# Kernel tuning notes

Measured on AMD Instinct MI355X. Metric: run time of the kernel, lower is better.

The kernel has to match this reference:

```python
import jax, jax.numpy as jnp
import numpy as np

WS = 4      # window_size
H = 128     # hidden_size
IN = 3      # input_size (1 control + 2 state channels)
OUT = 2     # out_size = input_size - 1


def _lstm_layer(x, Wih, Whh, b):
    # x: [B, S, Din] -> ys: [B, S, H], h/c: [B, H]. PyTorch gate order i,f,g,o.
    B = x.shape[0]
    xg = jnp.einsum('bsd,gd->bsg', x, Wih) + b  # precompute input projections

    def step(carry, xt):
        h, c = carry
        g = xt + h @ Whh.T
        i, f, gg, o = jnp.split(g, 4, axis=-1)
        c = jax.nn.sigmoid(f) * c + jax.nn.sigmoid(i) * jnp.tanh(gg)
        h = jax.nn.sigmoid(o) * jnp.tanh(c)
        return (h, c), h

    z = jnp.zeros((B, Whh.shape[1]), x.dtype)
    (h, c), ys = jax.lax.scan(step, (z, z), xg.transpose(1, 0, 2))
    return ys.transpose(1, 0, 2), h, c


def _lstm2(x, p):
    (Wih0, Whh0, b0), (Wih1, Whh1, b1) = p
    y0, h0, c0 = _lstm_layer(x, Wih0, Whh0, b0)
    y1, h1, c1 = _lstm_layer(y0, Wih1, Whh1, b1)
    return y1, jnp.stack([h0, h1]), jnp.stack([c0, c1])


def _forward(traj, Wih0, Whh0, bih0, bhh0, Wih1, Whh1, bih1, bhh1, Wl, bl):
    p = ((Wih0, Whh0, bih0 + bhh0), (Wih1, Whh1, bih1 + bhh1))
    head = lambda ys: ys[:, -1] @ Wl.T + bl  # linear applied to last LSTM step (== pred[:, -1])
    T = traj.shape[1]

    # initial window on raw trajectory
    ys, h, c = _lstm2(traj[:, :WS], p)
    out = traj[:, WS - 1:WS, 1:] + head(ys)[:, None, :]  # [B, 1, OUT]

    # warm-up phase: windows mix raw traj rows with predicted rows (features ordered [ctrl, out])
    for t in range(1, WS):
        tmp = jnp.concatenate([traj[:, WS + t:WS + t + 1, 0:1], out[:, t - 1:t, :]], axis=2)
        seq = jnp.concatenate([traj[:, t:WS + t - 1, :], tmp], axis=1)  # [B, WS, IN]
        ys, h, c = _lstm2(seq, p)
        out = jnp.concatenate([out, traj[:, WS + t - 1:WS + t, 1:] + head(ys)[:, None, :]], axis=1)

    nsteps = T - 2 * WS
    idx = WS + np.arange(nsteps)[:, None] + np.arange(WS)[None, :]  # [nsteps, WS]
    ctrl = traj[:, :, 0][:, idx].transpose(1, 0, 2)[..., None]      # [nsteps, B, WS, 1]

    def step(carry, ctrl_t):
        win, _, _ = carry
        seq = jnp.concatenate([win, ctrl_t], axis=2)  # [B, WS, OUT+1]
        ys, h, c = _lstm2(seq, p)
        new = win[:, -1, :] + head(ys)                # [B, OUT]
        win = jnp.concatenate([win[:, 1:], new[:, None, :]], axis=1)
        return (win, h, c), new

    (win, h, c), news = jax.lax.scan(step, (out, h, c), ctrl)
    out = jnp.concatenate([out, news.transpose(1, 0, 2)], axis=1)  # [B, T-WS, OUT]
    return out, h, c


def setup_inputs():
    key = jax.random.key(0)
    ks = jax.random.split(key, 11)
    B, T = 128, 256
    s = 1.0 / np.sqrt(H)
    u = lambda k, shp: jax.random.uniform(k, shp, jnp.float32, -s, s)
    return dict(
        one_full_traj=jax.random.normal(ks[0], (B, T, IN), jnp.float32),
        Wih0=u(ks[1], (4 * H, IN)), Whh0=u(ks[2], (4 * H, H)),
        bih0=u(ks[3], (4 * H,)), bhh0=u(ks[4], (4 * H,)),
        Wih1=u(ks[5], (4 * H, H)), Whh1=u(ks[6], (4 * H, H)),
        bih1=u(ks[7], (4 * H,)), bhh1=u(ks[8], (4 * H,)),
        Wl=u(ks[9], (OUT, H)), bl=u(ks[10], (OUT,)),
    )


def reference(one_full_traj, Wih0, Whh0, bih0, bhh0, Wih1, Whh1, bih1, bhh1, Wl, bl):
    # returns (out, h_n, c_n) matching torch's (out, hidden)
    return _forward(one_full_traj, Wih0, Whh0, bih0, bhh0, Wih1, Whh1, bih1, bhh1, Wl, bl)
```

## Files before the change

### kernel.cpp

```cpp
#include <hip/hip_runtime.h>

typedef _Float16 half2_t __attribute__((ext_vector_type(2)));
typedef unsigned int u32;

#define NW 252

__device__ inline u32 pk(float x, float y) {
  half2_t h; h.x = (_Float16)x; h.y = (_Float16)y;
  return __builtin_bit_cast(u32, h);
}

__device__ inline float fdot2(u32 a, u32 b, float c) {
#if __has_builtin(__builtin_amdgcn_fdot2)
  return __builtin_amdgcn_fdot2(__builtin_bit_cast(half2_t, a),
                                __builtin_bit_cast(half2_t, b), c, false);
#else
  half2_t ah = __builtin_bit_cast(half2_t, a);
  half2_t bh = __builtin_bit_cast(half2_t, b);
  return c + (float)ah.x * (float)bh.x + (float)ah.y * (float)bh.y;
#endif
}

__device__ inline float fast_rcp(float x) {
#if __has_builtin(__builtin_amdgcn_rcpf)
  return __builtin_amdgcn_rcpf(x);
#else
  return 1.0f / x;
#endif
}

__device__ inline float sigf(float x)  { return fast_rcp(1.0f + __expf(-x)); }
__device__ inline float tanh_(float x) { return 1.0f - 2.0f * fast_rcp(__expf(2.0f * x) + 1.0f); }

__device__ inline float quad_reduce(float v) {
  int x = __builtin_bit_cast(int, v);
  int y = __builtin_amdgcn_update_dpp(0, x, 0xB1, 0xF, 0xF, true);
  v += __builtin_bit_cast(float, y);
  x = __builtin_bit_cast(int, v);
  y = __builtin_amdgcn_update_dpp(0, x, 0x4E, 0xF, 0xF, true);
  v += __builtin_bit_cast(float, y);
  return v;
}

#define LOAD_SLICE(dst, basehalf)                                          \
  { const uint4* _p = (const uint4*)(basehalf) + ks * 4;                   \
    uint4 _q0 = _p[0], _q1 = _p[1], _q2 = _p[2], _q3 = _p[3];              \
    dst[0]=_q0.x;  dst[1]=_q0.y;  dst[2]=_q0.z;  dst[3]=_q0.w;             \
    dst[4]=_q1.x;  dst[5]=_q1.y;  dst[6]=_q1.z;  dst[7]=_q1.w;             \
    dst[8]=_q2.x;  dst[9]=_q2.y;  dst[10]=_q2.z; dst[11]=_q2.w;            \
    dst[12]=_q3.x; dst[13]=_q3.y; dst[14]=_q3.z; dst[15]=_q3.w; }

__global__ __launch_bounds__(512) void lstm_roll(
    const float* __restrict__ traj,
    const float* __restrict__ Wih0, const float* __restrict__ Whh0,
    const float* __restrict__ bih0, const float* __restrict__ bhh0,
    const float* __restrict__ Wih1, const float* __restrict__ Whh1,
    const float* __restrict__ bih1, const float* __restrict__ bhh1,
    const float* __restrict__ Wl,   const float* __restrict__ bl,
    float* __restrict__ out)
{
  const int b   = blockIdx.x;
  const int B   = gridDim.x;
  const int tid = threadIdx.x;
  const int j   = tid >> 2;
  const int ks  = tid & 3;

  __shared__ __align__(16) _Float16 h0buf[2][128];
  __shared__ __align__(16) _Float16 h1buf[2][128];
  __shared__ float sh_h1f[128];
  __shared__ float sh_Wl[256];
  __shared__ float trajS[256 * 3];
  __shared__ float preds[NW * 2];

  for (int i = tid; i < 768; i += 512) trajS[i] = traj[b * 768 + i];
  if (tid < 256) sh_Wl[tid] = Wl[tid];
  float blv = 0.0f;
  if (tid < 128) blv = bl[tid >> 6];

  u32 wA[64], wB[64], wC[64];
  float b0r[4], b1r[4], w0r[12];
#pragma unroll
  for (int g = 0; g < 4; ++g) {
    const int row = g * 128 + j;
    b0r[g] = bih0[row] + bhh0[row];
    b1r[g] = bih1[row] + bhh1[row];
    w0r[g*3+0] = Wih0[row*3+0];
    w0r[g*3+1] = Wih0[row*3+1];
    w0r[g*3+2] = Wih0[row*3+2];
    const float4* pA = (const float4*)(Whh0 + row * 128 + ks * 32);
    const float4* pB = (const float4*)(Wih1 + row * 128 + ks * 32);
    const float4* pC = (const float4*)(Whh1 + row * 128 + ks * 32);
#pragma unroll
    for (int q = 0; q < 8; ++q) {
      float4 fa = pA[q], fb = pB[q], fc = pC[q];
      wA[g*16 + q*2    ] = pk(fa.x, fa.y);
      wA[g*16 + q*2 + 1] = pk(fa.z, fa.w);
      wB[g*16 + q*2    ] = pk(fb.x, fb.y);
      wB[g*16 + q*2 + 1] = pk(fb.z, fb.w);
      wC[g*16 + q*2    ] = pk(fc.x, fc.y);
      wC[g*16 + q*2 + 1] = pk(fc.z, fc.w);
    }
  }

  float c0 = 0.f, c1 = 0.f, h0f = 0.f, h1f = 0.f;
  __syncthreads();

#pragma unroll 1
  for (int w = 0; w < NW; ++w) {
    c0 = 0.f; c1 = 0.f;
    for (int t = 0; t < 4; ++t) {
      float x0, x1, x2;
      if (w < 4) {
        if (w == 0 || t < 3) {
          const float* r = &trajS[(w + t) * 3];
          x0 = r[0]; x1 = r[1]; x2 = r[2];
        } else {
          x0 = trajS[(4 + w) * 3];
          x1 = preds[(w - 1) * 2];
          x2 = preds[(w - 1) * 2 + 1];
        }
      } else {
        const int s = w - 4;
        x0 = preds[(s + t) * 2];
        x1 = preds[(s + t) * 2 + 1];
        x2 = trajS[(4 + s + t) * 3];
      }
      const int rp = t & 1, wp = rp ^ 1;
      const bool lead = (ks == 0);

      float acc0, acc1, acc2, acc3;
      {
        float a0 = b0r[0] + w0r[0]*x0 + w0r[1] *x1 + w0r[2] *x2;
        float a1 = b0r[1] + w0r[3]*x0 + w0r[4] *x1 + w0r[5] *x2;
        float a2 = b0r[2] + w0r[6]*x0 + w0r[7] *x1 + w0r[8] *x2;
        float a3 = b0r[3] + w0r[9]*x0 + w0r[10]*x1 + w0r[11]*x2;
        acc0 = lead ? a0 : 0.f;  acc1 = lead ? a1 : 0.f;
        acc2 = lead ? a2 : 0.f;  acc3 = lead ? a3 : 0.f;
      }
      if (t > 0) {
        u32 su[16];
        LOAD_SLICE(su, h0buf[rp]);
#pragma unroll
        for (int kk = 0; kk < 16; ++kk) {
          acc0 = fdot2(wA[     kk], su[kk], acc0);
          acc1 = fdot2(wA[16 + kk], su[kk], acc1);
          acc2 = fdot2(wA[32 + kk], su[kk], acc2);
          acc3 = fdot2(wA[48 + kk], su[kk], acc3);
        }
      }
      acc0 = quad_reduce(acc0); acc1 = quad_reduce(acc1);
      acc2 = quad_reduce(acc2); acc3 = quad_reduce(acc3);
      {
        float ig = sigf(acc0), fg = sigf(acc1), gg = tanh_(acc2), og = sigf(acc3);
        c0  = fg * c0 + ig * gg;
        h0f = og * tanh_(c0);
      }
      if (lead) h0buf[wp][j] = (_Float16)h0f;
      __syncthreads();

      acc0 = lead ? b1r[0] : 0.f;  acc1 = lead ? b1r[1] : 0.f;
      acc2 = lead ? b1r[2] : 0.f;  acc3 = lead ? b1r[3] : 0.f;
      {
        u32 sy[16];
        LOAD_SLICE(sy, h0buf[wp]);
#pragma unroll
        for (int kk = 0; kk < 16; ++kk) {
          acc0 = fdot2(wB[     kk], sy[kk], acc0);
          acc1 = fdot2(wB[16 + kk], sy[kk], acc1);
          acc2 = fdot2(wB[32 + kk], sy[kk], acc2);
          acc3 = fdot2(wB[48 + kk], sy[kk], acc3);
        }
      }
      if (t > 0) {
        u32 sh[16];
        LOAD_SLICE(sh, h1buf[rp]);
#pragma unroll
        for (int kk = 0; kk < 16; ++kk) {
          acc0 = fdot2(wC[     kk], sh[kk], acc0);
          acc1 = fdot2(wC[16 + kk], sh[kk], acc1);
          acc2 = fdot2(wC[32 + kk], sh[kk], acc2);
          acc3 = fdot2(wC[48 + kk], sh[kk], acc3);
        }
      }
      acc0 = quad_reduce(acc0); acc1 = quad_reduce(acc1);
      acc2 = quad_reduce(acc2); acc3 = quad_reduce(acc3);
      {
        float ig = sigf(acc0), fg = sigf(acc1), gg = tanh_(acc2), og = sigf(acc3);
        c1  = fg * c1 + ig * gg;
        h1f = og * tanh_(c1);
      }
      if (lead) {
        h1buf[wp][j] = (_Float16)h1f;
        if (t == 3) sh_h1f[j] = h1f;
      }
      if (t == 3) __syncthreads();
    }

    if (tid < 128) {
      const int d = tid >> 6, l = tid & 63;
      float p = sh_Wl[d*128 + 2*l] * sh_h1f[2*l] + sh_Wl[d*128 + 2*l + 1] * sh_h1f[2*l + 1];
      p += __shfl_xor(p, 1);  p += __shfl_xor(p, 2);  p += __shfl_xor(p, 4);
      p += __shfl_xor(p, 8);  p += __shfl_xor(p, 16); p += __shfl_xor(p, 32);
      if (l == 0) {
        float base = (w < 4) ? trajS[(3 + w) * 3 + 1 + d] : preds[(w - 1) * 2 + d];
        preds[w * 2 + d] = base + p + blv;
      }
    }
    __syncthreads();
  }

  for (int i = tid; i < NW * 2; i += 512) out[b * (NW * 2) + i] = preds[i];
  if (ks == 0) {
    const int oh = B * NW * 2;
    const int oc = oh + 2 * B * 128;
    out[oh +            b * 128 + j] = h0f;
    out[oh + B * 128 +  b * 128 + j] = h1f;
    out[oc +            b * 128 + j] = c0;
    out[oc + B * 128 +  b * 128 + j] = c1;
  }
}

extern "C" void kernel_launch(void* const* d_in, const int* in_sizes, int n_in,
                              void* d_out, int out_size, void* d_ws, size_t ws_size,
                              hipStream_t stream) {
  const float* traj = (const float*)d_in[0];
  const float* Wih0 = (const float*)d_in[1];
  const float* Whh0 = (const float*)d_in[2];
  const float* bih0 = (const float*)d_in[3];
  const float* bhh0 = (const float*)d_in[4];
  const float* Wih1 = (const float*)d_in[5];
  const float* Whh1 = (const float*)d_in[6];
  const float* bih1 = (const float*)d_in[7];
  const float* bhh1 = (const float*)d_in[8];
  const float* Wl   = (const float*)d_in[9];
  const float* bl   = (const float*)d_in[10];

  const int B = in_sizes[0] / (256 * 3);
  hipLaunchKernelGGL(lstm_roll, dim3(B), dim3(512), 0, stream,
                     traj, Wih0, Whh0, bih0, bhh0, Wih1, Whh1, bih1, bhh1,
                     Wl, bl, (float*)d_out);
}
```

Measured before the change: 1.560 ms.

## Skew LSTM layers across time steps and defer head to cut barriers

Restructures the per-window loop as a wavefront. Layer-0 step t+1 now runs in the same barrier phase as layer-1 step t, and layer-0 step 0 of the next window is folded into the last phase of the current one. This cuts block-wide barriers per window from six to four. The linear head is moved to 8 threads using a quad reduce and deferred to the start of the next window, taking its separate barrier off the critical path. It also adds launch_bounds(512,2), which caps registers per thread while each thread keeps 192 packed weight registers, so spilling is a risk.

Result: faster. 1.328 ms (-14.9%).

```diff
diff --git a/kernel.cpp b/kernel.cpp
--- a/kernel.cpp
+++ b/kernel.cpp
@@ -50,7 +50,7 @@
     dst[8]=_q2.x;  dst[9]=_q2.y;  dst[10]=_q2.z; dst[11]=_q2.w;            \
     dst[12]=_q3.x; dst[13]=_q3.y; dst[14]=_q3.z; dst[15]=_q3.w; }
 
-__global__ __launch_bounds__(512) void lstm_roll(
+__global__ __launch_bounds__(512, 2) void lstm_roll(
     const float* __restrict__ traj,
     const float* __restrict__ Wih0, const float* __restrict__ Whh0,
     const float* __restrict__ bih0, const float* __restrict__ bhh0,
@@ -75,7 +75,7 @@
   for (int i = tid; i < 768; i += 512) trajS[i] = traj[b * 768 + i];
   if (tid < 256) sh_Wl[tid] = Wl[tid];
   float blv = 0.0f;
-  if (tid < 128) blv = bl[tid >> 6];
+  if (tid < 8) blv = bl[tid >> 2];
 
   u32 wA[64], wB[64], wC[64];
   float b0r[4], b1r[4], w0r[12];
@@ -103,111 +103,130 @@
   }
 
   float c0 = 0.f, c1 = 0.f, h0f = 0.f, h1f = 0.f;
+
+  auto L0STEP = [&](int w_, int t_, int p_) {
+    float x0, x1, x2;
+    if (w_ < 4) {
+      if (w_ == 0 || t_ < 3) {
+        const float* r = &trajS[(w_ + t_) * 3];
+        x0 = r[0]; x1 = r[1]; x2 = r[2];
+      } else {
+        x0 = trajS[(4 + w_) * 3];
+        x1 = preds[(w_ - 1) * 2];
+        x2 = preds[(w_ - 1) * 2 + 1];
+      }
+    } else {
+      const int s_ = w_ - 4;
+      x0 = preds[(s_ + t_) * 2];
+      x1 = preds[(s_ + t_) * 2 + 1];
+      x2 = trajS[(w_ + t_) * 3];
+    }
+    const bool lead = (ks == 0);
+    float a0 = b0r[0] + w0r[0]*x0 + w0r[1] *x1 + w0r[2] *x2;
+    float a1 = b0r[1] + w0r[3]*x0 + w0r[4] *x1 + w0r[5] *x2;
+    float a2 = b0r[2] + w0r[6]*x0 + w0r[7] *x1 + w0r[8] *x2;
+    float a3 = b0r[3] + w0r[9]*x0 + w0r[10]*x1 + w0r[11]*x2;
+    float acc0 = lead ? a0 : 0.f, acc1 = lead ? a1 : 0.f;
+    float acc2 = lead ? a2 : 0.f, acc3 = lead ? a3 : 0.f;
+    if (t_ > 0) {
+      u32 su[16];
+      LOAD_SLICE(su, h0buf[p_]);
+#pragma unroll
+      for (int kk = 0; kk < 16; ++kk) {
+        acc0 = fdot2(wA[     kk], su[kk], acc0);
+        acc1 = fdot2(wA[16 + kk], su[kk], acc1);
+        acc2 = fdot2(wA[32 + kk], su[kk], acc2);
+        acc3 = fdot2(wA[48 + kk], su[kk], acc3);
+      }
+    }
+    acc0 = quad_reduce(acc0); acc1 = quad_reduce(acc1);
+    acc2 = quad_reduce(acc2); acc3 = quad_reduce(acc3);
+    float ig = sigf(acc0), fg = sigf(acc1), gg = tanh_(acc2), og = sigf(acc3);
+    float cp = t_ ? c0 : 0.f;
+    c0  = fg * cp + ig * gg;
+    h0f = og * tanh_(c0);
+    if (lead) h0buf[p_ ^ 1][j] = (_Float16)h0f;
+  };
+
+  auto L1STEP = [&](int t_, int p_) {
+    const bool lead = (ks == 0);
+    float acc0 = lead ? b1r[0] : 0.f, acc1 = lead ? b1r[1] : 0.f;
+    float acc2 = lead ? b1r[2] : 0.f, acc3 = lead ? b1r[3] : 0.f;
+    {
+      u32 sy[16];
+      LOAD_SLICE(sy, h0buf[p_]);
+#pragma unroll
+      for (int kk = 0; kk < 16; ++kk) {
+        acc0 = fdot2(wB[     kk], sy[kk], acc0);
+        acc1 = fdot2(wB[16 + kk], sy[kk], acc1);
+        acc2 = fdot2(wB[32 + kk], sy[kk], acc2);
+        acc3 = fdot2(wB[48 + kk], sy[kk], acc3);
+      }
+    }
+    if (t_ > 0) {
+      u32 sh[16];
+      LOAD_SLICE(sh, h1buf[p_]);
+#pragma unroll
+      for (int kk = 0; kk < 16; ++kk) {
+        acc0 = fdot2(wC[     kk], sh[kk], acc0);
+        acc1 = fdot2(wC[16 + kk], sh[kk], acc1);
+        acc2 = fdot2(wC[32 + kk], sh[kk], acc2);
+        acc3 = fdot2(wC[48 + kk], sh[kk], acc3);
+      }
+    }
+    acc0 = quad_reduce(acc0); acc1 = quad_reduce(acc1);
+    acc2 = quad_reduce(acc2); acc3 = quad_reduce(acc3);
+    float ig = sigf(acc0), fg = sigf(acc1), gg = tanh_(acc2), og = sigf(acc3);
+    float cp = t_ ? c1 : 0.f;
+    c1  = fg * cp + ig * gg;
+    h1f = og * tanh_(c1);
+    if (lead) {
+      h1buf[p_ ^ 1][j] = (_Float16)h1f;
+      if (t_ == 3) sh_h1f[j] = h1f;
+    }
+  };
+
+  auto HD = [&](int w_) {
+    if (tid < 8) {
+      const int d = tid >> 2;
+      const float* wrow = &sh_Wl[d * 128 + ks * 32];
+      const float* hrow = &sh_h1f[ks * 32];
+      float s = 0.f;
+#pragma unroll
+      for (int m = 0; m < 32; ++m) s = fmaf(wrow[m], hrow[m], s);
+      s = quad_reduce(s);
+      if (ks == 0) {
+        float base = (w_ < 4) ? trajS[(3 + w_) * 3 + 1 + d] : preds[(w_ - 1) * 2 + d];
+        preds[w_ * 2 + d] = base + s + blv;
+      }
+    }
+  };
+
   __syncthreads();
+
+  int p = 0;
+  L0STEP(0, 0, p);
+  __syncthreads(); p ^= 1;
 
 #pragma unroll 1
   for (int w = 0; w < NW; ++w) {
-    c0 = 0.f; c1 = 0.f;
-    for (int t = 0; t < 4; ++t) {
-      float x0, x1, x2;
-      if (w < 4) {
-        if (w == 0 || t < 3) {
-          const float* r = &trajS[(w + t) * 3];
-          x0 = r[0]; x1 = r[1]; x2 = r[2];
-        } else {
-          x0 = trajS[(4 + w) * 3];
-          x1 = preds[(w - 1) * 2];
-          x2 = preds[(w - 1) * 2 + 1];
-        }
-      } else {
-        const int s = w - 4;
-        x0 = preds[(s + t) * 2];
-        x1 = preds[(s + t) * 2 + 1];
-        x2 = trajS[(4 + s + t) * 3];
-      }
-      const int rp = t & 1, wp = rp ^ 1;
-      const bool lead = (ks == 0);
-
-      float acc0, acc1, acc2, acc3;
-      {
-        float a0 = b0r[0] + w0r[0]*x0 + w0r[1] *x1 + w0r[2] *x2;
-        float a1 = b0r[1] + w0r[3]*x0 + w0r[4] *x1 + w0r[5] *x2;
-        float a2 = b0r[2] + w0r[6]*x0 + w0r[7] *x1 + w0r[8] *x2;
-        float a3 = b0r[3] + w0r[9]*x0 + w0r[10]*x1 + w0r[11]*x2;
-        acc0 = lead ? a0 : 0.f;  acc1 = lead ? a1 : 0.f;
-        acc2 = lead ? a2 : 0.f;  acc3 = lead ? a3 : 0.f;
-      }
-      if (t > 0) {
-        u32 su[16];
-        LOAD_SLICE(su, h0buf[rp]);
-#pragma unroll
-        for (int kk = 0; kk < 16; ++kk) {
-          acc0 = fdot2(wA[     kk], su[kk], acc0);
-          acc1 = fdot2(wA[16 + kk], su[kk], acc1);
-          acc2 = fdot2(wA[32 + kk], su[kk], acc2);
-          acc3 = fdot2(wA[48 + kk], su[kk], acc3);
-        }
-      }
-      acc0 = quad_reduce(acc0); acc1 = quad_reduce(acc1);
-      acc2 = quad_reduce(acc2); acc3 = quad_reduce(acc3);
-      {
-        float ig = sigf(acc0), fg = sigf(acc1), gg = tanh_(acc2), og = sigf(acc3);
-        c0  = fg * c0 + ig * gg;
-        h0f = og * tanh_(c0);
-      }
-      if (lead) h0buf[wp][j] = (_Float16)h0f;
-      __syncthreads();
-
-      acc0 = lead ? b1r[0] : 0.f;  acc1 = lead ? b1r[1] : 0.f;
-      acc2 = lead ? b1r[2] : 0.f;  acc3 = lead ? b1r[3] : 0.f;
-      {
-        u32 sy[16];
-        LOAD_SLICE(sy, h0buf[wp]);
-#pragma unroll
-        for (int kk = 0; kk < 16; ++kk) {
-          acc0 = fdot2(wB[     kk], sy[kk], acc0);
-          acc1 = fdot2(wB[16 + kk], sy[kk], acc1);
-          acc2 = fdot2(wB[32 + kk], sy[kk], acc2);
-          acc3 = fdot2(wB[48 + kk], sy[kk], acc3);
-        }
-      }
-      if (t > 0) {
-        u32 sh[16];
-        LOAD_SLICE(sh, h1buf[rp]);
-#pragma unroll
-        for (int kk = 0; kk < 16; ++kk) {
-          acc0 = fdot2(wC[     kk], sh[kk], acc0);
-          acc1 = fdot2(wC[16 + kk], sh[kk], acc1);
-          acc2 = fdot2(wC[32 + kk], sh[kk], acc2);
-          acc3 = fdot2(wC[48 + kk], sh[kk], acc3);
-        }
-      }
-      acc0 = quad_reduce(acc0); acc1 = quad_reduce(acc1);
-      acc2 = quad_reduce(acc2); acc3 = quad_reduce(acc3);
-      {
-        float ig = sigf(acc0), fg = sigf(acc1), gg = tanh_(acc2), og = sigf(acc3);
-        c1  = fg * c1 + ig * gg;
-        h1f = og * tanh_(c1);
-      }
-      if (lead) {
-        h1buf[wp][j] = (_Float16)h1f;
-        if (t == 3) sh_h1f[j] = h1f;
-      }
-      if (t == 3) __syncthreads();
-    }
-
-    if (tid < 128) {
-      const int d = tid >> 6, l = tid & 63;
-      float p = sh_Wl[d*128 + 2*l] * sh_h1f[2*l] + sh_Wl[d*128 + 2*l + 1] * sh_h1f[2*l + 1];
-      p += __shfl_xor(p, 1);  p += __shfl_xor(p, 2);  p += __shfl_xor(p, 4);
-      p += __shfl_xor(p, 8);  p += __shfl_xor(p, 16); p += __shfl_xor(p, 32);
-      if (l == 0) {
-        float base = (w < 4) ? trajS[(3 + w) * 3 + 1 + d] : preds[(w - 1) * 2 + d];
-        preds[w * 2 + d] = base + p + blv;
-      }
-    }
-    __syncthreads();
+    if (w > 0) HD(w - 1);
+    L0STEP(w, 1, p);
+    L1STEP(0, p);
+    __syncthreads(); p ^= 1;
+    L0STEP(w, 2, p);
+    L1STEP(1, p);
+    __syncthreads(); p ^= 1;
+    L0STEP(w, 3, p);
+    L1STEP(2, p);
+    __syncthreads(); p ^= 1;
+    L1STEP(3, p);
+    if (w < NW - 1) L0STEP(w + 1, 0, p);
+    __syncthreads(); p ^= 1;
   }
+
+  HD(NW - 1);
+  __syncthreads();
 
   for (int i = tid; i < NW * 2; i += 512) out[b * (NW * 2) + i] = preds[i];
   if (ks == 0) {
```
